# Performance work log

Hardware: AMD Instinct MI355X
Metric: run time of the kernel (lower is better)

Reference implementation:

```python
import jax, jax.numpy as jnp
import numpy as np

NEG = -1e30  # stands in for float('-inf') masking; kept finite for safe grads


def setup_inputs() -> dict:
    key = jax.random.key(0)
    k1, k2 = jax.random.split(key)
    B, T, C = 256, 16, 2048
    return {
        "seq_features1": jax.random.normal(k1, (B, T, C), dtype=jnp.float32),
        "seq_features2": jax.random.normal(k2, (B, T, C), dtype=jnp.float32),
    }


def _cpa_dp(f1, f2):
    """Faithful translation of the CPA_learnStep DP core: similarity softmax ->
    2D cumsum -> 5D block/area tensors -> sequential max+gather recurrence."""
    B, T, C = f1.shape
    scores = jnp.einsum('bic,bjc->bij', f1, f2) / jnp.sqrt(jnp.asarray(C, f1.dtype))
    pred = jax.nn.softmax(scores, axis=-1)
    pred = jnp.cumsum(jnp.cumsum(pred, axis=-2), axis=-1)  # [B,T,T]

    idx1 = jnp.arange(T, dtype=pred.dtype) + 1.0
    denom = idx1[:, None] * idx1[None, :]                  # (i+1)*(j+1), [T,T]
    D0 = pred / denom                                      # D[:,0]

    # area[i,j,a,b] = denom[i,j] - denom[i,b] - denom[a,j] + denom[a,b]
    area = (denom[:, :, None, None] - denom[:, None, None, :]
            - denom[None, :, :, None] + denom[None, None, :, :])
    area = jnp.sqrt(jnp.maximum(area, 1.0))                # clamp_min(1).sqrt()

    # block[b,i,j,a,bb] = pred[b,i,j] - pred[b,i,bb] - pred[b,a,j] + pred[b,a,bb]
    block = (pred[:, :, :, None, None] - pred[:, :, None, None, :]
             - jnp.swapaxes(pred, 1, 2)[:, None, :, :, None]
             + pred[:, None, None, :, :])
    ar = jnp.arange(T)
    # mask where (a >= i) | (b >= j)
    mask = ((ar[None, None, :, None] >= ar[:, None, None, None]) |
            (ar[None, None, None, :] >= ar[None, :, None, None]))  # [T,T,T,T]
    block = jnp.where(mask[None], jnp.asarray(NEG, block.dtype), block) / area[None]
    blockf = block.reshape(B, T, T, T * T)                 # flatten (a,bb)

    def step(D_prev, _):
        # tmp[b,i,j,(a,bb)] = D_prev[b,a,bb] + block[b,i,j,a,bb]
        flat = D_prev.reshape(B, 1, 1, T * T) + blockf
        D_k = jnp.max(flat, axis=-1)                       # [B,T,T]
        ind = jnp.argmax(flat, axis=-1)                    # [B,T,T]
        blk = jnp.take_along_axis(blockf, ind[..., None], axis=-1)[..., 0]
        return D_k, (D_k[:, T - 1, T - 1], ind, blk)

    _, (fin_tail, D_ind, D_block) = jax.lax.scan(step, D0, None, length=T - 1)

    # final_result[b,k] = D[b,k,T-1,T-1]
    final_result = jnp.concatenate([D0[None, :, T - 1, T - 1], fin_tail], axis=0).T  # [B,T]
    loss_step = -jnp.max(final_result, axis=-1)
    step_num = jnp.argmax(final_result, axis=-1)
    return loss_step, step_num, D_ind, D_block


def reference(seq_features1, seq_features2):
    loss_step, step_num, D_ind, D_block = _cpa_dp(seq_features1, seq_features2)
    return loss_step, step_num
```

## Files before the change

kernel.cpp:

```cpp
#include <hip/hip_runtime.h>
#include <math.h>

#define TT 16
#define CC 2048
#define NEGV -1.0e30f
#define CW 256
#define NCK (CC / CW)
#define ASTR 260
#define SSTR 17
#define PSTR 48
#define DSTR 48

#define KEEP(x) asm volatile("" : "+v"(x))

#define RORF(dst, src, n)                                                      \
    dst = __int_as_float(__builtin_amdgcn_update_dpp(                          \
        0, __float_as_int(src), 0x120 + (n), 0xF, 0xF, false))

__global__ __launch_bounds__(1024, 1) void cpa_kernel(
    const float* __restrict__ f1, const float* __restrict__ f2,
    float* __restrict__ out, int B)
{
    __shared__ float  As[TT * ASTR];
    __shared__ float  Bs[TT * ASTR];
    __shared__ float4 part4[256];
    __shared__ float  Ps[TT * SSTR];
    __shared__ float  Pq[TT * SSTR];
    __shared__ float  Pm[TT * PSTR];
    __shared__ float  Dm[2 * TT * DSTR];
    __shared__ float  fin[TT];

    const int b    = blockIdx.x;
    const int tid  = threadIdx.x;
    const int wv   = tid >> 6;
    const int lane = tid & 63;

    const int ti = wv >> 2, tj = wv & 3;
    const float* baseA = f1 + (size_t)b * TT * CC;
    const float* baseB = f2 + (size_t)b * TT * CC;

    float4 av = *(const float4*)(baseA + wv * CC + lane * 4);
    float4 bv = *(const float4*)(baseB + wv * CC + lane * 4);

    float acc[4][4] = {};
    for (int ck = 0; ck < NCK; ++ck) {
        *(float4*)&As[wv * ASTR + lane * 4] = av;
        *(float4*)&Bs[wv * ASTR + lane * 4] = bv;
        __syncthreads();
        if (ck + 1 < NCK) {
            av = *(const float4*)(baseA + wv * CC + (ck + 1) * CW + lane * 4);
            bv = *(const float4*)(baseB + wv * CC + (ck + 1) * CW + lane * 4);
        }
        float4 bn[4];
        #pragma unroll
        for (int n = 0; n < 4; ++n)
            bn[n] = *(const float4*)&Bs[(tj * 4 + n) * ASTR + lane * 4];
        #pragma unroll
        for (int m = 0; m < 4; ++m) {
            float4 am = *(const float4*)&As[(ti * 4 + m) * ASTR + lane * 4];
            #pragma unroll
            for (int n = 0; n < 4; ++n) {
                acc[m][n] = fmaf(am.x, bn[n].x, acc[m][n]);
                acc[m][n] = fmaf(am.y, bn[n].y, acc[m][n]);
                acc[m][n] = fmaf(am.z, bn[n].z, acc[m][n]);
                acc[m][n] = fmaf(am.w, bn[n].w, acc[m][n]);
            }
        }
        __syncthreads();
    }
    #pragma unroll
    for (int m = 0; m < 4; ++m) {
        #pragma unroll
        for (int n = 0; n < 4; ++n) {
            float v = acc[m][n], t;
            RORF(t, v, 1); v += t;
            RORF(t, v, 2); v += t;
            RORF(t, v, 4); v += t;
            RORF(t, v, 8); v += t;
            if ((lane & 15) == 0)
                ((float*)&part4[(ti * 4 + m) * 16 + (tj * 4 + n)])[lane >> 4] = v;
        }
    }
    __syncthreads();

    if (tid < 256) {
        const int si = tid >> 4, sj = tid & 15;
        float4 p = part4[tid];
        float s = (p.x + p.y + p.z + p.w) * (1.0f / sqrtf((float)CC));
        float mx = s;
        #pragma unroll
        for (int d = 1; d < 16; d <<= 1) mx = fmaxf(mx, __shfl_xor(mx, d));
        const float e = expf(s - mx);
        float sm = e;
        #pragma unroll
        for (int d = 1; d < 16; d <<= 1) sm += __shfl_xor(sm, d);
        Ps[si * SSTR + sj] = e / sm;
    }
    __syncthreads();

    if (tid < 256) {
        const int r = tid >> 4, c = tid & 15;
        float run = Ps[c];
        #pragma unroll
        for (int rr = 1; rr < TT; ++rr)
            if (rr <= r) run += Ps[rr * SSTR + c];
        Pq[r * SSTR + c] = run;
    }
    __syncthreads();
    if (tid < 256) {
        const int r = tid >> 4, c = tid & 15;
        float run = Pq[r * SSTR];
        #pragma unroll
        for (int cc = 1; cc < TT; ++cc)
            if (cc <= c) run += Pq[r * SSTR + cc];
        Pm[r * PSTR + c] = run;
    }
    __syncthreads();

    const int i_dp = (int)((0x612073458ABC9DEFull >> (4 * wv)) & 15);
    const int ksD  = lane >> 4;
    const int j    = lane & 15;
    const float jf = (float)j;

    const float pij = Pm[i_dp * PSTR + j];
    float vA0 = Pm[(ksD +  0) * PSTR + j];
    float vA1 = Pm[(ksD +  4) * PSTR + j];
    float vA2 = Pm[(ksD +  8) * PSTR + j];
    float vA3 = Pm[(ksD + 12) * PSTR + j];
    float ca0, ca1, ca2, ca3, ra0, ra1, ra2, ra3;
    {
        int a, d1;
        a = ksD;      ca0 = -vA0 + (a < i_dp ? 0.f : NEGV); d1 = i_dp - a; if (d1 < 1) d1 = 1; ra0 = rsqrtf((float)d1);
        a = ksD + 4;  ca1 = -vA1 + (a < i_dp ? 0.f : NEGV); d1 = i_dp - a; if (d1 < 1) d1 = 1; ra1 = rsqrtf((float)d1);
        a = ksD + 8;  ca2 = -vA2 + (a < i_dp ? 0.f : NEGV); d1 = i_dp - a; if (d1 < 1) d1 = 1; ra2 = rsqrtf((float)d1);
        a = ksD + 12; ca3 = -vA3 + (a < i_dp ? 0.f : NEGV); d1 = i_dp - a; if (d1 < 1) d1 = 1; ra3 = rsqrtf((float)d1);
    }

    float qr[4][16];
    qr[0][0] = (ca0 + NEGV + vA0) * ra0; KEEP(qr[0][0]);
    qr[1][0] = (ca1 + NEGV + vA1) * ra1; KEEP(qr[1][0]);
    qr[2][0] = (ca2 + NEGV + vA2) * ra2; KEEP(qr[2][0]);
    qr[3][0] = (ca3 + NEGV + vA3) * ra3; KEEP(qr[3][0]);

#define QSTEP(n)                                                               \
    {                                                                          \
        float bbf, rIt, rAt;                                                   \
        RORF(bbf, jf, n);                                                      \
        RORF(rIt, pij, n);                                                     \
        const int bbi = (int)bbf;                                              \
        int d2 = j - bbi; if (d2 < 1) d2 = 1;                                  \
        const float rjt = rsqrtf((float)d2);                                   \
        const float cbm = pij - rIt + ((bbi < j) ? 0.0f : NEGV);               \
        RORF(rAt, vA0, n); qr[0][n] = (ca0 + cbm + rAt) * (ra0 * rjt); KEEP(qr[0][n]); \
        RORF(rAt, vA1, n); qr[1][n] = (ca1 + cbm + rAt) * (ra1 * rjt); KEEP(qr[1][n]); \
        RORF(rAt, vA2, n); qr[2][n] = (ca2 + cbm + rAt) * (ra2 * rjt); KEEP(qr[2][n]); \
        RORF(rAt, vA3, n); qr[3][n] = (ca3 + cbm + rAt) * (ra3 * rjt); KEEP(qr[3][n]); \
    }
    QSTEP(1)  QSTEP(2)  QSTEP(3)  QSTEP(4)  QSTEP(5)  QSTEP(6)  QSTEP(7)
    QSTEP(8)  QSTEP(9)  QSTEP(10) QSTEP(11) QSTEP(12) QSTEP(13) QSTEP(14) QSTEP(15)
#undef QSTEP

    const float D0 = pij / (float)((i_dp + 1) * (j + 1));
    if (ksD == 0) Dm[i_dp * DSTR + j] = D0;
    if (wv == 0 && lane == 15) fin[0] = D0;
    __syncthreads();

    const int nA = (i_dp + 3) >> 2;

#define DSTEP(A_, n, MACC)                                                     \
    { float dt_; RORF(dt_, dbase, n); MACC = fmaxf(MACC, dt_ + qr[A_][n]); }
#define AABLOCK(A_, TLO_, NM_)                                                 \
    if (A_ >= (TLO_) && A_ < nA) {                                             \
        const float dbase = Dold[(ksD + A_ * 4) * DSTR + j];                   \
        m0 = fmaxf(m0, dbase + qr[A_][0]);                                     \
        if (1  <= (NM_)) DSTEP(A_, 1, m1)                                      \
        if (2  <= (NM_)) DSTEP(A_, 2, m2)                                      \
        if (3  <= (NM_)) DSTEP(A_, 3, m3)                                      \
        if (4  <= (NM_)) DSTEP(A_, 4, m0)                                      \
        if (5  <= (NM_)) DSTEP(A_, 5, m1)                                      \
        if (6  <= (NM_)) DSTEP(A_, 6, m2)                                      \
        if (7  <= (NM_)) DSTEP(A_, 7, m3)                                      \
        if (8  <= (NM_)) DSTEP(A_, 8, m0)                                      \
        if (9  <= (NM_)) DSTEP(A_, 9, m1)                                      \
        if (10 <= (NM_)) DSTEP(A_, 10, m2)                                     \
        if (11 <= (NM_)) DSTEP(A_, 11, m3)                                     \
        if (12 <= (NM_)) DSTEP(A_, 12, m0)                                     \
        if (13 <= (NM_)) DSTEP(A_, 13, m1)                                     \
        if (14 <= (NM_)) DSTEP(A_, 14, m2)                                     \
        if (15 <= (NM_)) DSTEP(A_, 15, m3)                                     \
    }

    #pragma unroll
    for (int k = 1; k < TT; ++k) {
        const float* Dold = Dm + ((k - 1) & 1) * (TT * DSTR);
        float*       Dnew = Dm + (k & 1)       * (TT * DSTR);
        if (i_dp >= k) {
            const int tlo  = (k - 1) >> 2;
            const int nmax = 16 - k;
            float m0 = -3.0e38f, m1 = -3.0e38f, m2 = -3.0e38f, m3 = -3.0e38f;
            AABLOCK(0, tlo, nmax)
            AABLOCK(1, tlo, nmax)
            AABLOCK(2, tlo, nmax)
            AABLOCK(3, tlo, nmax)
            float mm = fmaxf(fmaxf(m0, m1), fmaxf(m2, m3));
            mm = fmaxf(mm, __shfl_xor(mm, 16));
            mm = fmaxf(mm, __shfl_xor(mm, 32));
            if (ksD == 0) Dnew[i_dp * DSTR + j] = mm;
            if (wv == 0 && lane == 15) fin[k] = mm;
        } else if (ksD == 0) {
            Dnew[i_dp * DSTR + j] = -3.0e38f;
        }
        __syncthreads();
    }
#undef AABLOCK
#undef DSTEP

    if (tid == 0) {
        float best = fin[0];
        int   idx  = 0;
        #pragma unroll
        for (int k = 1; k < TT; ++k) {
            if (fin[k] > best) { best = fin[k]; idx = k; }
        }
        out[b]     = -best;
        out[B + b] = (float)idx;
    }
}

extern "C" void kernel_launch(void* const* d_in, const int* in_sizes, int n_in,
                              void* d_out, int out_size, void* d_ws, size_t ws_size,
                              hipStream_t stream)
{
    const float* f1 = (const float*)d_in[0];
    const float* f2 = (const float*)d_in[1];
    float* out = (float*)d_out;
    const int B = in_sizes[0] / (TT * CC);
    hipLaunchKernelGGL(cpa_kernel, dim3(B), dim3(1024), 0, stream, f1, f2, out, B);
}
```

Baseline: 29.13 us.

## Split channel reduction across blocks into separate partial-GEMM kernel

```diff
diff --git a/kernel.cpp b/kernel.cpp
--- a/kernel.cpp
+++ b/kernel.cpp
@@ -17,9 +17,65 @@
     dst = __int_as_float(__builtin_amdgcn_update_dpp(                          \
         0, __float_as_int(src), 0x120 + (n), 0xF, 0xF, false))
 
-__global__ __launch_bounds__(1024, 1) void cpa_kernel(
+__global__ __launch_bounds__(1024, 1) void gemm_part(
     const float* __restrict__ f1, const float* __restrict__ f2,
-    float* __restrict__ out, int B)
+    float* __restrict__ ws, int B)
+{
+    __shared__ float As[TT * ASTR];
+    __shared__ float Bs[TT * ASTR];
+
+    const int b    = blockIdx.x;
+    const int s    = blockIdx.y;
+    const int tid  = threadIdx.x;
+    const int wv   = tid >> 6;
+    const int lane = tid & 63;
+    const int ti   = wv >> 2, tj = wv & 3;
+
+    const float* baseA = f1 + (size_t)b * TT * CC + s * CW;
+    const float* baseB = f2 + (size_t)b * TT * CC + s * CW;
+
+    *(float4*)&As[wv * ASTR + lane * 4] = *(const float4*)(baseA + wv * CC + lane * 4);
+    *(float4*)&Bs[wv * ASTR + lane * 4] = *(const float4*)(baseB + wv * CC + lane * 4);
+    __syncthreads();
+
+    float4 bn[4];
+    #pragma unroll
+    for (int n = 0; n < 4; ++n)
+        bn[n] = *(const float4*)&Bs[(tj * 4 + n) * ASTR + lane * 4];
+    float acc[4][4] = {};
+    #pragma unroll
+    for (int m = 0; m < 4; ++m) {
+        float4 am = *(const float4*)&As[(ti * 4 + m) * ASTR + lane * 4];
+        #pragma unroll
+        for (int n = 0; n < 4; ++n) {
+            acc[m][n] = fmaf(am.x, bn[n].x, acc[m][n]);
+            acc[m][n] = fmaf(am.y, bn[n].y, acc[m][n]);
+            acc[m][n] = fmaf(am.z, bn[n].z, acc[m][n]);
+            acc[m][n] = fmaf(am.w, bn[n].w, acc[m][n]);
+        }
+    }
+    float* wsb = ws + ((size_t)s * B + b) * 256;
+    #pragma unroll
+    for (int m = 0; m < 4; ++m) {
+        #pragma unroll
+        for (int n = 0; n < 4; ++n) {
+            float v = acc[m][n], t;
+            RORF(t, v, 1); v += t;
+            RORF(t, v, 2); v += t;
+            RORF(t, v, 4); v += t;
+            RORF(t, v, 8); v += t;
+            v += __shfl_xor(v, 16);
+            v += __shfl_xor(v, 32);
+            if (lane == 0)
+                wsb[(ti * 4 + m) * 16 + (tj * 4 + n)] = v;
+        }
+    }
+}
+
+template <bool SPLIT>
+__global__ __launch_bounds__(1024, 1) void cpa_main(
+    const float* __restrict__ f1, const float* __restrict__ f2,
+    const float* __restrict__ ws, float* __restrict__ out, int B)
 {
     __shared__ float  As[TT * ASTR];
     __shared__ float  Bs[TT * ASTR];
@@ -35,58 +91,69 @@
     const int wv   = tid >> 6;
     const int lane = tid & 63;
 
-    const int ti = wv >> 2, tj = wv & 3;
-    const float* baseA = f1 + (size_t)b * TT * CC;
-    const float* baseB = f2 + (size_t)b * TT * CC;
-
-    float4 av = *(const float4*)(baseA + wv * CC + lane * 4);
-    float4 bv = *(const float4*)(baseB + wv * CC + lane * 4);
-
-    float acc[4][4] = {};
-    for (int ck = 0; ck < NCK; ++ck) {
-        *(float4*)&As[wv * ASTR + lane * 4] = av;
-        *(float4*)&Bs[wv * ASTR + lane * 4] = bv;
-        __syncthreads();
-        if (ck + 1 < NCK) {
-            av = *(const float4*)(baseA + wv * CC + (ck + 1) * CW + lane * 4);
-            bv = *(const float4*)(baseB + wv * CC + (ck + 1) * CW + lane * 4);
-        }
-        float4 bn[4];
-        #pragma unroll
-        for (int n = 0; n < 4; ++n)
-            bn[n] = *(const float4*)&Bs[(tj * 4 + n) * ASTR + lane * 4];
+    if (!SPLIT) {
+        const int ti = wv >> 2, tj = wv & 3;
+        const float* baseA = f1 + (size_t)b * TT * CC;
+        const float* baseB = f2 + (size_t)b * TT * CC;
+
+        float4 av = *(const float4*)(baseA + wv * CC + lane * 4);
+        float4 bv = *(const float4*)(baseB + wv * CC + lane * 4);
+
+        float acc[4][4] = {};
+        for (int ck = 0; ck < NCK; ++ck) {
+            *(float4*)&As[wv * ASTR + lane * 4] = av;
+            *(float4*)&Bs[wv * ASTR + lane * 4] = bv;
+            __syncthreads();
+            if (ck + 1 < NCK) {
+                av = *(const float4*)(baseA + wv * CC + (ck + 1) * CW + lane * 4);
+                bv = *(const float4*)(baseB + wv * CC + (ck + 1) * CW + lane * 4);
+            }
+            float4 bn[4];
+            #pragma unroll
+            for (int n = 0; n < 4; ++n)
+                bn[n] = *(const float4*)&Bs[(tj * 4 + n) * ASTR + lane * 4];
+            #pragma unroll
+            for (int m = 0; m < 4; ++m) {
+                float4 am = *(const float4*)&As[(ti * 4 + m) * ASTR + lane * 4];
+                #pragma unroll
+                for (int n = 0; n < 4; ++n) {
+                    acc[m][n] = fmaf(am.x, bn[n].x, acc[m][n]);
+                    acc[m][n] = fmaf(am.y, bn[n].y, acc[m][n]);
+                    acc[m][n] = fmaf(am.z, bn[n].z, acc[m][n]);
+                    acc[m][n] = fmaf(am.w, bn[n].w, acc[m][n]);
+                }
+            }
+            __syncthreads();
+        }
         #pragma unroll
         for (int m = 0; m < 4; ++m) {
-            float4 am = *(const float4*)&As[(ti * 4 + m) * ASTR + lane * 4];
             #pragma unroll
             for (int n = 0; n < 4; ++n) {
-                acc[m][n] = fmaf(am.x, bn[n].x, acc[m][n]);
-                acc[m][n] = fmaf(am.y, bn[n].y, acc[m][n]);
-                acc[m][n] = fmaf(am.z, bn[n].z, acc[m][n]);
-                acc[m][n] = fmaf(am.w, bn[n].w, acc[m][n]);
+                float v = acc[m][n], t;
+                RORF(t, v, 1); v += t;
+                RORF(t, v, 2); v += t;
+                RORF(t, v, 4); v += t;
+                RORF(t, v, 8); v += t;
+                if ((lane & 15) == 0)
+                    ((float*)&part4[(ti * 4 + m) * 16 + (tj * 4 + n)])[lane >> 4] = v;
             }
         }
         __syncthreads();
     }
-    #pragma unroll
-    for (int m = 0; m < 4; ++m) {
-        #pragma unroll
-        for (int n = 0; n < 4; ++n) {
-            float v = acc[m][n], t;
-            RORF(t, v, 1); v += t;
-            RORF(t, v, 2); v += t;
-            RORF(t, v, 4); v += t;
-            RORF(t, v, 8); v += t;
-            if ((lane & 15) == 0)
-                ((float*)&part4[(ti * 4 + m) * 16 + (tj * 4 + n)])[lane >> 4] = v;
-        }
-    }
-    __syncthreads();
 
     if (tid < 256) {
         const int si = tid >> 4, sj = tid & 15;
-        float4 p = part4[tid];
-        float s = (p.x + p.y + p.z + p.w) * (1.0f / sqrtf((float)CC));
+        float s;
+        if (SPLIT) {
+            s = 0.f;
+            #pragma unroll
+            for (int sl = 0; sl < NCK; ++sl)
+                s += ws[((size_t)sl * B + b) * 256 + tid];
+        } else {
+            float4 p = part4[tid];
+            s = p.x + p.y + p.z + p.w;
+        }
+        s *= (1.0f / sqrtf((float)CC));
         float mx = s;
         #pragma unroll
         for (int d = 1; d < 16; d <<= 1) mx = fmaxf(mx, __shfl_xor(mx, d));
@@ -235,5 +302,15 @@
     const float* f2 = (const float*)d_in[1];
     float* out = (float*)d_out;
     const int B = in_sizes[0] / (TT * CC);
-    hipLaunchKernelGGL(cpa_kernel, dim3(B), dim3(1024), 0, stream, f1, f2, out, B);
+    const size_t need = (size_t)NCK * B * 256 * sizeof(float);
+    if (ws_size >= need) {
+        float* ws = (float*)d_ws;
+        hipLaunchKernelGGL(gemm_part, dim3(B, NCK), dim3(1024), 0, stream,
+                           f1, f2, ws, B);
+        hipLaunchKernelGGL((cpa_main<true>), dim3(B), dim3(1024), 0, stream,
+                           f1, f2, (const float*)ws, out, B);
+    } else {
+        hipLaunchKernelGGL((cpa_main<false>), dim3(B), dim3(1024), 0, stream,
+                           f1, f2, (const float*)nullptr, out, B);
+    }
 }
```

New measurement: 37.13 us. 27.5% more time.
